# Optimization experiments

Hardware: AMD Instinct MI355X
Metric: run time of the kernel (lower is better)

## Reference

```python
import jax, jax.numpy as jnp
import numpy as np

N_NODES = 100000
N_EDGES = 1600000
D = 128
L = 3


def setup_inputs() -> dict:
    key = jax.random.key(0)
    k1, k2, k3 = jax.random.split(key, 3)
    edge_index = jax.random.randint(k1, (2, N_EDGES), 0, N_NODES, dtype=jnp.int64)
    emb = jax.random.normal(k2, (N_NODES, D), dtype=jnp.float32)
    # Glorot-style scale for the per-layer linear weights
    Ws = jax.random.normal(k3, (L, D, D), dtype=jnp.float32) * (1.0 / np.sqrt(D))
    bs = jnp.zeros((L, D), dtype=jnp.float32)
    return {"edge_index": edge_index, "emb": emb, "Ws": Ws, "bs": bs}


def _gcn_forward(emb, Ws, bs, edge_index):
    n = emb.shape[0]
    self_loop = jnp.arange(n, dtype=edge_index.dtype)
    # PyG GCNConv adds self-loops and uses symmetric normalization
    row = jnp.concatenate([edge_index[0], self_loop])  # source nodes
    col = jnp.concatenate([edge_index[1], self_loop])  # target nodes
    deg = jax.ops.segment_sum(jnp.ones(row.shape[0], dtype=emb.dtype), col, num_segments=n)
    deg_inv_sqrt = jnp.where(deg > 0, jax.lax.rsqrt(jnp.maximum(deg, 1.0)), 0.0)
    norm = deg_inv_sqrt[row] * deg_inv_sqrt[col]  # [E+N]

    x = emb
    for l in range(Ws.shape[0]):
        h = x @ Ws[l]                              # [N, D] linear transform
        msg = h[row] * norm[:, None]               # gather + scale [E+N, D]
        x = jax.ops.segment_sum(msg, col, num_segments=n) + bs[l]  # scatter-add
        x = jax.nn.relu(x)                         # dropout is identity in eval
    return x


def reference(edge_index, emb, Ws, bs) -> jnp.ndarray:
    return _gcn_forward(emb, Ws, bs, edge_index)
```

## Files before the change

### kernel.cpp

```cpp
#include <hip/hip_runtime.h>
#include <hip/hip_fp16.h>
#include <cstdint>
#include <cstddef>

#define N_NODES 100000
#define N_EDGES 1600000
#define D 128
#define NLAYERS 3
#define NB 3125
#define NBLK_E 128
#define EPB 12500
#define ENT_CAP 1024

typedef float f2v __attribute__((ext_vector_type(2)));
typedef float f4v __attribute__((ext_vector_type(4)));


__global__ __launch_bounds__(512) void hist1_kernel(const int* __restrict__ col,
                                                    int* __restrict__ hmat) {
    __shared__ int hist[NB];
    int b = blockIdx.x, t = threadIdx.x;
    for (int j = t; j < NB; j += 512) hist[j] = 0;
    __syncthreads();
    int base = b * EPB;
    for (int i = t; i < EPB; i += 512) {
        int c = col[base + i];
        atomicAdd(&hist[c >> 5], 1);
    }
    __syncthreads();
    for (int j = t; j < NB; j += 512) hmat[b * NB + j] = hist[j];
}

__global__ void btot_kernel(const int* __restrict__ hmat, int* __restrict__ btot) {
    int j = blockIdx.x * 256 + threadIdx.x;
    if (j < NB) {
        int s = 0;
        for (int b = 0; b < NBLK_E; b++) s += hmat[b * NB + j];
        btot[j] = s;
    }
}

__global__ void bscan_kernel(const int* __restrict__ btot, int* __restrict__ bstart, int nb, int e) {
    __shared__ int lsum[1024];
    int t = threadIdx.x;
    int vals[4];
    int v0 = 0;
#pragma unroll
    for (int j = 0; j < 4; j++) {
        int idx = t * 4 + j;
        int c = (idx < nb) ? btot[idx] : 0;
        vals[j] = c;
        v0 += c;
    }
    lsum[t] = v0;
    __syncthreads();
    for (int off = 1; off < 1024; off <<= 1) {
        int x = (t >= off) ? lsum[t - off] : 0;
        __syncthreads();
        lsum[t] += x;
        __syncthreads();
    }
    int base = lsum[t] - v0;
#pragma unroll
    for (int j = 0; j < 4; j++) {
        int idx = t * 4 + j;
        if (idx < nb) {
            bstart[idx] = base;
            base += vals[j];
        }
    }
    if (t == 0) bstart[nb] = e;
}

__global__ void hoff_kernel(const int* __restrict__ hmat, const int* __restrict__ bstart,
                            int* __restrict__ hoff) {
    int j = blockIdx.x * 256 + threadIdx.x;
    if (j < NB) {
        int run = bstart[j];
        for (int b = 0; b < NBLK_E; b++) {
            hoff[b * NB + j] = run;
            run += hmat[b * NB + j];
        }
    }
}

__global__ __launch_bounds__(512) void scatter_kernel(const int* __restrict__ row,
                                                      const int* __restrict__ col,
                                                      const int* __restrict__ hoff,
                                                      unsigned* __restrict__ bucketbuf) {
    __shared__ int cur[NB];
    int b = blockIdx.x, t = threadIdx.x;
    for (int j = t; j < NB; j += 512) cur[j] = hoff[b * NB + j];
    __syncthreads();
    int base = b * EPB;
    for (int i = t; i < EPB; i += 512) {
        int r = row[base + i], c = col[base + i];
        int pos = atomicAdd(&cur[c >> 5], 1);
        bucketbuf[pos] = ((unsigned)r << 5) | (unsigned)(c & 31);
    }
}

__global__ void fill2_kernel(const unsigned* __restrict__ bucketbuf, const int* __restrict__ bstart,
                             int* __restrict__ offsets, float* __restrict__ dinv,
                             int* __restrict__ src, int n, int e) {
    __shared__ unsigned ent[ENT_CAP];
    __shared__ int hist[32];
    __shared__ int cur[32];
    __shared__ int loff[32];
    int b = blockIdx.x, t = threadIdx.x;
    int s0 = bstart[b];
    int cnt = bstart[b + 1] - s0;
    if (cnt > ENT_CAP) cnt = ENT_CAP;
    if (t < 32) hist[t] = 0;
    __syncthreads();
    for (int i = t; i < cnt; i += 256) {
        unsigned v = bucketbuf[s0 + i];
        ent[i] = v;
        atomicAdd(&hist[v & 31], 1);
    }
    __syncthreads();
    if (t == 0) {
        int run = s0;
#pragma unroll
        for (int j = 0; j < 32; j++) {
            loff[j] = run;
            run += hist[j];
        }
    }
    __syncthreads();
    if (t < 32) {
        int node = b * 32 + t;
        int o = loff[t];
        offsets[node] = o;
        cur[t] = o;
        dinv[node] = rsqrtf((float)(hist[t] + 1));
    }
    if (b == 0 && t == 0) offsets[n] = e;
    __syncthreads();
    for (int i = t; i < cnt; i += 256) {
        unsigned v = ent[i];
        int pos = atomicAdd(&cur[v & 31], 1);
        src[pos] = (int)(v >> 5);
    }
}


__global__ void cast_kernel(const float2* __restrict__ in, const float* __restrict__ dinv,
                            __half2* __restrict__ out, int n2) {
    int i = blockIdx.x * 256 + threadIdx.x;
    if (i < n2) {
        float d = dinv[i >> 6];
        float2 v = in[i];
        out[i] = __floats2half2_rn(d * v.x, d * v.y);
    }
}

__global__ void agg_kernel(const __half2* __restrict__ xs, const int* __restrict__ offs,
                           float* __restrict__ out, const float* __restrict__ dinv,
                           const int* __restrict__ src) {
    int v = blockIdx.x;
    int f = threadIdx.x;
    float dv = dinv[v];
    float2 a0 = __half22float2(xs[(size_t)v * 64 + f]);
    float ax = a0.x;
    float ay = a0.y;
    int i = offs[v], s1 = offs[v + 1];
    for (; i + 7 < s1; i += 8) {
        int s[8];
#pragma unroll
        for (int j = 0; j < 8; j++) s[j] = src[i + j];
        float2 x[8];
#pragma unroll
        for (int j = 0; j < 8; j++) x[j] = __half22float2(xs[(size_t)s[j] * 64 + f]);
#pragma unroll
        for (int j = 0; j < 8; j++) {
            ax += x[j].x;
            ay += x[j].y;
        }
    }
    if (i < s1) {
        int last = s1 - 1;
        int s[8];
        float m[8];
#pragma unroll
        for (int j = 0; j < 8; j++) {
            int idx = i + j;
            bool in = idx < s1;
            s[j] = src[in ? idx : last];
            m[j] = in ? 1.0f : 0.0f;
        }
        float2 x[8];
#pragma unroll
        for (int j = 0; j < 8; j++) x[j] = __half22float2(xs[(size_t)s[j] * 64 + f]);
#pragma unroll
        for (int j = 0; j < 8; j++) {
            ax += m[j] * x[j].x;
            ay += m[j] * x[j].y;
        }
    }
    f2v r;
    r.x = dv * ax;
    r.y = dv * ay;
    __builtin_nontemporal_store(r, (f2v*)out + (size_t)v * 64 + f);
}

__global__ __launch_bounds__(256, 2) void gemm_bias_relu_kernel(
    const float* __restrict__ A, const float* __restrict__ W,
    const float* __restrict__ bias, float* __restrict__ out,
    __half2* __restrict__ xs_out, const float* __restrict__ dinv,
    int write_h, int write_out) {
    __shared__ float sW[128 * 128];
    __shared__ float sX[32 * 128];
    int t = threadIdx.x;
    int tx = t & 31;
    int ty = t >> 5;
    int row0 = blockIdx.x * 32;

    const f4v* W4 = (const f4v*)W;
    f4v* sW4 = (f4v*)sW;
#pragma unroll
    for (int i = 0; i < 16; i++) sW4[t + 256 * i] = W4[t + 256 * i];

    const f4v* A4 = (const f4v*)A;
    f4v* sX4 = (f4v*)sX;
#pragma unroll
    for (int i = 0; i < 4; i++) {
        int c = t + 256 * i;
        int r = c >> 5, kc = c & 31;
        sX4[r * 32 + kc] = __builtin_nontemporal_load(&A4[(size_t)(row0 + r) * 32 + kc]);
    }
    __syncthreads();

    float4 acc[4];
#pragma unroll
    for (int r = 0; r < 4; r++) acc[r] = make_float4(0.f, 0.f, 0.f, 0.f);

#define FMA4(a, s, b) a.x += (s) * (b).x; a.y += (s) * (b).y; a.z += (s) * (b).z; a.w += (s) * (b).w;
#pragma unroll 4
    for (int k0 = 0; k0 < 128; k0 += 4) {
        float4 b0 = *(const float4*)&sW[(k0 + 0) * 128 + tx * 4];
        float4 b1 = *(const float4*)&sW[(k0 + 1) * 128 + tx * 4];
        float4 b2 = *(const float4*)&sW[(k0 + 2) * 128 + tx * 4];
        float4 b3 = *(const float4*)&sW[(k0 + 3) * 128 + tx * 4];
#pragma unroll
        for (int r = 0; r < 4; r++) {
            float4 a = *(const float4*)&sX[(ty * 4 + r) * 128 + k0];
            FMA4(acc[r], a.x, b0)
            FMA4(acc[r], a.y, b1)
            FMA4(acc[r], a.z, b2)
            FMA4(acc[r], a.w, b3)
        }
    }
#undef FMA4

    float4 bb = ((const float4*)bias)[tx];
#pragma unroll
    for (int r = 0; r < 4; r++) {
        float4 o;
        o.x = fmaxf(acc[r].x + bb.x, 0.0f);
        o.y = fmaxf(acc[r].y + bb.y, 0.0f);
        o.z = fmaxf(acc[r].z + bb.z, 0.0f);
        o.w = fmaxf(acc[r].w + bb.w, 0.0f);
        size_t rowi = (size_t)(row0 + ty * 4 + r);
        if (write_out) {
            f4v ov;
            ov.x = o.x; ov.y = o.y; ov.z = o.z; ov.w = o.w;
            __builtin_nontemporal_store(ov, (f4v*)out + rowi * 32 + tx);
        }
        if (write_h) {
            float dr = dinv[rowi];
            xs_out[rowi * 64 + tx * 2] = __floats2half2_rn(dr * o.x, dr * o.y);
            xs_out[rowi * 64 + tx * 2 + 1] = __floats2half2_rn(dr * o.z, dr * o.w);
        }
    }
}


extern "C" void kernel_launch(void* const* d_in, const int* in_sizes, int n_in,
                              void* d_out, int out_size, void* d_ws, size_t ws_size,
                              hipStream_t stream) {
    const int* edge = (const int*)d_in[0];
    const float* emb = (const float*)d_in[1];
    const float* Ws = (const float*)d_in[2];
    const float* bs = (const float*)d_in[3];
    float* out = (float*)d_out;

    const int n = N_NODES, e = N_EDGES;
    const int* row = edge;
    const int* col = edge + e;

    char* p = (char*)d_ws;
    float* aggbuf = (float*)p;
    int* hmat = (int*)p;
    int* hoff = hmat + (size_t)NBLK_E * NB;
    p += (size_t)n * D * 4;
    __half2* xs = (__half2*)p;
    unsigned* bucketbuf = (unsigned*)p;
    p += (size_t)n * D * 2;
    int* csr_src  = (int*)p;    p += (size_t)e * 4;
    float* dinv   = (float*)p;  p += (size_t)n * 4;
    int* offsets  = (int*)p;    p += (size_t)(n + 1) * 4;
    int* btot     = (int*)p;    p += (size_t)NB * 4;
    int* bstart   = (int*)p;    p += (size_t)(NB + 1) * 4;

    hist1_kernel<<<NBLK_E, 512, 0, stream>>>(col, hmat);
    btot_kernel<<<(NB + 255) / 256, 256, 0, stream>>>(hmat, btot);
    bscan_kernel<<<1, 1024, 0, stream>>>(btot, bstart, NB, e);
    hoff_kernel<<<(NB + 255) / 256, 256, 0, stream>>>(hmat, bstart, hoff);
    scatter_kernel<<<NBLK_E, 512, 0, stream>>>(row, col, hoff, bucketbuf);
    fill2_kernel<<<NB, 256, 0, stream>>>(bucketbuf, bstart, offsets, dinv, csr_src, n, e);

    int n2 = n * 64;
    cast_kernel<<<(n2 + 255) / 256, 256, 0, stream>>>((const float2*)emb, dinv, xs, n2);

    for (int l = 0; l < NLAYERS; l++) {
        agg_kernel<<<n, 64, 0, stream>>>(xs, offsets, aggbuf, dinv, csr_src);
        gemm_bias_relu_kernel<<<n / 32, 256, 0, stream>>>(
            aggbuf, Ws + (size_t)l * D * D, bs + (size_t)l * D, out,
            xs, dinv,
            (l < NLAYERS - 1) ? 1 : 0, (l == NLAYERS - 1) ? 1 : 0);
    }
}
```

Before: 530.1 us.

## Retile GEMM to 128-row blocks with K-chunked W and 8x8 register tiles

Rewrites the dense GEMM+bias+ReLU kernel to process 128 rows per block, streaming W and A through shared memory in 32-wide K chunks. Each thread now computes an 8x8 output tile using transposed, XOR-swizzled A in LDS. This raises arithmetic intensity and cuts the per-block reload of the full 64KB W. The aggregation buffer is padded to a multiple of 128 rows, and out-of-range rows are skipped at store time. The fp16 output stores are widened to 16-byte writes. Padded rows read uninitialized workspace data, which is harmless only because their results are discarded.

```diff
diff --git a/kernel.cpp b/kernel.cpp
--- a/kernel.cpp
+++ b/kernel.cpp
@@ -4,6 +4,7 @@
 #include <cstddef>
 
 #define N_NODES 100000
+#define N_PAD 100096
 #define N_EDGES 1600000
 #define D 128
 #define NLAYERS 3
@@ -204,73 +205,93 @@
     __builtin_nontemporal_store(r, (f2v*)out + (size_t)v * 64 + f);
 }
 
-__global__ __launch_bounds__(256, 2) void gemm_bias_relu_kernel(
+__global__ __launch_bounds__(256) void gemm_bias_relu_kernel(
     const float* __restrict__ A, const float* __restrict__ W,
     const float* __restrict__ bias, float* __restrict__ out,
     __half2* __restrict__ xs_out, const float* __restrict__ dinv,
-    int write_h, int write_out) {
-    __shared__ float sW[128 * 128];
-    __shared__ float sX[32 * 128];
+    int write_h, int write_out, int n) {
+    __shared__ float sA[32 * 128];
+    __shared__ float sW[32 * 128];
     int t = threadIdx.x;
-    int tx = t & 31;
-    int ty = t >> 5;
-    int row0 = blockIdx.x * 32;
-
-    const f4v* W4 = (const f4v*)W;
-    f4v* sW4 = (f4v*)sW;
-#pragma unroll
-    for (int i = 0; i < 16; i++) sW4[t + 256 * i] = W4[t + 256 * i];
+    int tx = t & 15;
+    int ty = t >> 4;
+    int row0 = blockIdx.x * 128;
+
+    f4v acc[8][2];
+#pragma unroll
+    for (int r = 0; r < 8; r++) {
+        acc[r][0] = (f4v){0.f, 0.f, 0.f, 0.f};
+        acc[r][1] = (f4v){0.f, 0.f, 0.f, 0.f};
+    }
 
     const f4v* A4 = (const f4v*)A;
-    f4v* sX4 = (f4v*)sX;
-#pragma unroll
-    for (int i = 0; i < 4; i++) {
-        int c = t + 256 * i;
-        int r = c >> 5, kc = c & 31;
-        sX4[r * 32 + kc] = __builtin_nontemporal_load(&A4[(size_t)(row0 + r) * 32 + kc]);
-    }
-    __syncthreads();
-
-    float4 acc[4];
-#pragma unroll
-    for (int r = 0; r < 4; r++) acc[r] = make_float4(0.f, 0.f, 0.f, 0.f);
-
-#define FMA4(a, s, b) a.x += (s) * (b).x; a.y += (s) * (b).y; a.z += (s) * (b).z; a.w += (s) * (b).w;
-#pragma unroll 4
-    for (int k0 = 0; k0 < 128; k0 += 4) {
-        float4 b0 = *(const float4*)&sW[(k0 + 0) * 128 + tx * 4];
-        float4 b1 = *(const float4*)&sW[(k0 + 1) * 128 + tx * 4];
-        float4 b2 = *(const float4*)&sW[(k0 + 2) * 128 + tx * 4];
-        float4 b3 = *(const float4*)&sW[(k0 + 3) * 128 + tx * 4];
-#pragma unroll
-        for (int r = 0; r < 4; r++) {
-            float4 a = *(const float4*)&sX[(ty * 4 + r) * 128 + k0];
-            FMA4(acc[r], a.x, b0)
-            FMA4(acc[r], a.y, b1)
-            FMA4(acc[r], a.z, b2)
-            FMA4(acc[r], a.w, b3)
-        }
-    }
-#undef FMA4
-
-    float4 bb = ((const float4*)bias)[tx];
-#pragma unroll
-    for (int r = 0; r < 4; r++) {
-        float4 o;
-        o.x = fmaxf(acc[r].x + bb.x, 0.0f);
-        o.y = fmaxf(acc[r].y + bb.y, 0.0f);
-        o.z = fmaxf(acc[r].z + bb.z, 0.0f);
-        o.w = fmaxf(acc[r].w + bb.w, 0.0f);
-        size_t rowi = (size_t)(row0 + ty * 4 + r);
+
+    for (int kc = 0; kc < 4; kc++) {
+        int kb = kc * 32;
+        {
+            const f4v* Wg = (const f4v*)(W + (size_t)kb * 128);
+            f4v* sW4 = (f4v*)sW;
+#pragma unroll
+            for (int i = 0; i < 4; i++) sW4[t + 256 * i] = Wg[t + 256 * i];
+        }
+#pragma unroll
+        for (int i = 0; i < 4; i++) {
+            int idx = t + 256 * i;
+            int r = idx >> 3;
+            int q = idx & 7;
+            f4v v = __builtin_nontemporal_load(&A4[(size_t)(row0 + r) * 32 + kc * 8 + q]);
+            int k0 = q * 4;
+            sA[(k0 + 0) * 128 + (r ^ ((k0 + 0) & 24))] = v.x;
+            sA[(k0 + 1) * 128 + (r ^ ((k0 + 1) & 24))] = v.y;
+            sA[(k0 + 2) * 128 + (r ^ ((k0 + 2) & 24))] = v.z;
+            sA[(k0 + 3) * 128 + (r ^ ((k0 + 3) & 24))] = v.w;
+        }
+        __syncthreads();
+
+#pragma unroll 8
+        for (int k = 0; k < 32; k++) {
+            const float* ap = &sA[k * 128 + ((ty * 8) ^ (k & 24))];
+            f4v a0 = *(const f4v*)ap;
+            f4v a1 = *(const f4v*)(ap + 4);
+            const float* bp = &sW[k * 128 + tx * 8];
+            f4v b0 = *(const f4v*)bp;
+            f4v b1 = *(const f4v*)(bp + 4);
+#pragma unroll
+            for (int r = 0; r < 4; r++) {
+                acc[r][0] += a0[r] * b0;
+                acc[r][1] += a0[r] * b1;
+                acc[r + 4][0] += a1[r] * b0;
+                acc[r + 4][1] += a1[r] * b1;
+            }
+        }
+        __syncthreads();
+    }
+
+    f4v bb0 = ((const f4v*)bias)[tx * 2];
+    f4v bb1 = ((const f4v*)bias)[tx * 2 + 1];
+#pragma unroll
+    for (int r = 0; r < 8; r++) {
+        int rowi = row0 + ty * 8 + r;
+        if (rowi >= n) continue;
+        f4v o0 = acc[r][0] + bb0;
+        f4v o1 = acc[r][1] + bb1;
+#pragma unroll
+        for (int j = 0; j < 4; j++) {
+            o0[j] = fmaxf(o0[j], 0.0f);
+            o1[j] = fmaxf(o1[j], 0.0f);
+        }
         if (write_out) {
-            f4v ov;
-            ov.x = o.x; ov.y = o.y; ov.z = o.z; ov.w = o.w;
-            __builtin_nontemporal_store(ov, (f4v*)out + rowi * 32 + tx);
+            __builtin_nontemporal_store(o0, (f4v*)out + (size_t)rowi * 32 + tx * 2);
+            __builtin_nontemporal_store(o1, (f4v*)out + (size_t)rowi * 32 + tx * 2 + 1);
         }
         if (write_h) {
             float dr = dinv[rowi];
-            xs_out[rowi * 64 + tx * 2] = __floats2half2_rn(dr * o.x, dr * o.y);
-            xs_out[rowi * 64 + tx * 2 + 1] = __floats2half2_rn(dr * o.z, dr * o.w);
+            __half2 h[4];
+            h[0] = __floats2half2_rn(dr * o0[0], dr * o0[1]);
+            h[1] = __floats2half2_rn(dr * o0[2], dr * o0[3]);
+            h[2] = __floats2half2_rn(dr * o1[0], dr * o1[1]);
+            h[3] = __floats2half2_rn(dr * o1[2], dr * o1[3]);
+            *(uint4*)&xs_out[(size_t)rowi * 64 + tx * 4] = *(uint4*)h;
         }
     }
 }
@@ -293,7 +314,7 @@
     float* aggbuf = (float*)p;
     int* hmat = (int*)p;
     int* hoff = hmat + (size_t)NBLK_E * NB;
-    p += (size_t)n * D * 4;
+    p += (size_t)N_PAD * D * 4;
     __half2* xs = (__half2*)p;
     unsigned* bucketbuf = (unsigned*)p;
     p += (size_t)n * D * 2;
@@ -313,11 +334,12 @@
     int n2 = n * 64;
     cast_kernel<<<(n2 + 255) / 256, 256, 0, stream>>>((const float2*)emb, dinv, xs, n2);
 
+    const int ngb = N_PAD / 128;
     for (int l = 0; l < NLAYERS; l++) {
         agg_kernel<<<n, 64, 0, stream>>>(xs, offsets, aggbuf, dinv, csr_src);
-        gemm_bias_relu_kernel<<<n / 32, 256, 0, stream>>>(
+        gemm_bias_relu_kernel<<<ngb, 256, 0, stream>>>(
             aggbuf, Ws + (size_t)l * D * D, bs + (size_t)l * D, out,
             xs, dinv,
-            (l < NLAYERS - 1) ? 1 : 0, (l == NLAYERS - 1) ? 1 : 0);
-    }
-}
+            (l < NLAYERS - 1) ? 1 : 0, (l == NLAYERS - 1) ? 1 : 0, n);
+    }
+}
```

Result: no change. 525.5 us (-0.9%).
